# Kernel optimization log

Hardware: AMD Instinct MI355X
Metric: run time of the kernel (lower is better)

Reference implementation:

```python
import jax, jax.numpy as jnp
import numpy as np

EMB, HID, VOC, NLAYERS, TLEN = 256, 512, 32000, 2, 64
SRC_LEN, BS = 128, 64
DEC_HID = 2 * HID  # decoder hidden = hidden_dim * 2


def _p(key, shape, scale=0.05):
    return jax.random.normal(key, shape, dtype=jnp.float32) * scale


def setup_inputs() -> dict:
    key = jax.random.key(0)
    ks = jax.random.split(key, 24)
    d = {}
    d["sentences"] = jax.random.randint(ks[0], (SRC_LEN, BS), 0, VOC)
    d["targets"] = jax.random.randint(ks[1], (TLEN, BS), 0, VOC)
    d["emb"] = _p(ks[2], (VOC, EMB))
    # encoder: bidirectional, 2 layers; gate order i,f,g,o (PyTorch)
    d["enc0_Wih"] = _p(ks[3], (2, 4 * HID, EMB))
    d["enc0_Whh"] = _p(ks[4], (2, 4 * HID, HID))
    d["enc0_bih"] = _p(ks[5], (2, 4 * HID))
    d["enc0_bhh"] = _p(ks[6], (2, 4 * HID))
    d["enc1_Wih"] = _p(ks[7], (2, 4 * HID, 2 * HID))
    d["enc1_Whh"] = _p(ks[8], (2, 4 * HID, HID))
    d["enc1_bih"] = _p(ks[9], (2, 4 * HID))
    d["enc1_bhh"] = _p(ks[10], (2, 4 * HID))
    # decoder: unidirectional, 2 layers, hidden DEC_HID
    d["dec0_Wih"] = _p(ks[11], (4 * DEC_HID, EMB))
    d["dec0_Whh"] = _p(ks[12], (4 * DEC_HID, DEC_HID))
    d["dec0_bih"] = _p(ks[13], (4 * DEC_HID,))
    d["dec0_bhh"] = _p(ks[14], (4 * DEC_HID,))
    d["dec1_Wih"] = _p(ks[15], (4 * DEC_HID, DEC_HID))
    d["dec1_Whh"] = _p(ks[16], (4 * DEC_HID, DEC_HID))
    d["dec1_bih"] = _p(ks[17], (4 * DEC_HID,))
    d["dec1_bhh"] = _p(ks[18], (4 * DEC_HID,))
    d["W_out"] = _p(ks[19], (VOC, DEC_HID))
    d["b_out"] = _p(ks[20], (VOC,))
    return d


def lstm_scan(x, h0, c0, Wih, Whh, bih, bhh, reverse=False):
    # x: (T,B,In). Precompute input projection for the whole sequence.
    xw = jnp.einsum('tbi,gi->tbg', x, Wih) + bih  # (T,B,4H)

    def step(carry, g_in):
        h, c = carry
        g = g_in + h @ Whh.T + bhh
        i, f, gg, o = jnp.split(g, 4, axis=-1)
        c = jax.nn.sigmoid(f) * c + jax.nn.sigmoid(i) * jnp.tanh(gg)
        h = jax.nn.sigmoid(o) * jnp.tanh(c)
        return (h, c), h

    (hT, cT), ys = jax.lax.scan(step, (h0, c0), xw, reverse=reverse)
    return ys, hT, cT


def _forward(sentences, targets, emb,
             enc0_Wih, enc0_Whh, enc0_bih, enc0_bhh,
             enc1_Wih, enc1_Whh, enc1_bih, enc1_bhh,
             dec0_Wih, dec0_Whh, dec0_bih, dec0_bhh,
             dec1_Wih, dec1_Whh, dec1_bih, dec1_bhh,
             W_out, b_out):
    bs = sentences.shape[1]
    x = emb[sentences]  # (S,B,E)
    z = jnp.zeros((bs, HID), jnp.float32)
    enc_layers = ((enc0_Wih, enc0_Whh, enc0_bih, enc0_bhh),
                  (enc1_Wih, enc1_Whh, enc1_bih, enc1_bhh))
    hs, cs = [], []
    for Wih, Whh, bih, bhh in enc_layers:
        yf, hf, cf = lstm_scan(x, z, z, Wih[0], Whh[0], bih[0], bhh[0])
        yb, hb, cb = lstm_scan(x, z, z, Wih[1], Whh[1], bih[1], bhh[1], reverse=True)
        x = jnp.concatenate([yf, yb], axis=-1)  # (S,B,2H)
        hs.append(jnp.concatenate([hf, hb], axis=-1))  # _reshape_hidden concat
        cs.append(jnp.concatenate([cf, cb], axis=-1))
    # teacher forcing: decoder inputs are last source token, then targets[:-1]
    dec_tokens = jnp.concatenate([sentences[-1:], targets[:-1]], axis=0)  # (T,B)
    y = emb[dec_tokens]  # (T,B,E); dropout is identity in eval mode
    dec_layers = ((dec0_Wih, dec0_Whh, dec0_bih, dec0_bhh),
                  (dec1_Wih, dec1_Whh, dec1_bih, dec1_bhh))
    for l, (Wih, Whh, bih, bhh) in enumerate(dec_layers):
        y, _, _ = lstm_scan(y, hs[l], cs[l], Wih, Whh, bih, bhh)
    logits = jnp.einsum('tbh,vh->tbv', y, W_out) + b_out  # (T,B,V)
    return jax.nn.log_softmax(logits, axis=-1)


def reference(sentences, targets, emb,
              enc0_Wih, enc0_Whh, enc0_bih, enc0_bhh,
              enc1_Wih, enc1_Whh, enc1_bih, enc1_bhh,
              dec0_Wih, dec0_Whh, dec0_bih, dec0_bhh,
              dec1_Wih, dec1_Whh, dec1_bih, dec1_bhh,
              W_out, b_out):
    return _forward(sentences, targets, emb,
                    enc0_Wih, enc0_Whh, enc0_bih, enc0_bhh,
                    enc1_Wih, enc1_Whh, enc1_bih, enc1_bhh,
                    dec0_Wih, dec0_Whh, dec0_bih, dec0_bhh,
                    dec1_Wih, dec1_Whh, dec1_bih, dec1_bhh,
                    W_out, b_out)
```

## Files before the change

### kernel.cpp

```cpp
#include <hip/hip_runtime.h>

#define S_LEN 128
#define T_LEN 64
#define BSZ   64
#define EMBD  256
#define HID_  512
#define DHID_ 1024
#define VOC_  32000
#define HSTR  1024

typedef float  f4_t  __attribute__((ext_vector_type(4)));
typedef float  f32x4 __attribute__((ext_vector_type(4)));
typedef short  s16x8 __attribute__((ext_vector_type(8)));
typedef __bf16 bf16x8 __attribute__((ext_vector_type(8)));
typedef unsigned short u16x4 __attribute__((ext_vector_type(4)));
typedef int    i32x2 __attribute__((ext_vector_type(2)));

#define WS_XWA  0ull
#define WS_XWB  (WS_XWA + 16777216ull)
#define WS_CS   (WS_XWB + 16777216ull)
#define WS_BAR  (WS_CS  + 131072ull)
#define WS_BF   (WS_BAR + 32768ull)
#define U_X0B   0ull
#define U_HE0   (U_X0B + 2097152ull)
#define U_HE1   (U_HE0 + 8388608ull)
#define U_HD0   (U_HE1 + 8388608ull)
#define U_HD1   (U_HD0 + 4194304ull)
#define U_HSB   (U_HD1 + 4194304ull)
#define U_E0W   (U_HSB + 131072ull)
#define U_E1W   (U_E0W + 1048576ull)
#define U_D0W   (U_E1W + 4194304ull)
#define U_D1W   (U_D0W + 1048576ull)

__device__ __forceinline__ unsigned short f2bf(float x) {
    unsigned u = __builtin_bit_cast(unsigned, x);
    return (unsigned short)((u + 0x7fffu + ((u >> 16) & 1u)) >> 16);
}

__device__ __forceinline__ f4_t sc_load4(const void* p) {
    f4_t v;
    asm volatile("global_load_dwordx4 %0, %1, off sc0 sc1" : "=v"(v) : "v"(p));
    return v;
}
__device__ __forceinline__ int sc_load1(const int* p) {
    int v;
    asm volatile("global_load_dword %0, %1, off sc0 sc1\n\ts_waitcnt vmcnt(0)"
                 : "=v"(v) : "v"(p) : "memory");
    return v;
}
__device__ __forceinline__ void sc_store_int(int* p, int v) {
    asm volatile("global_store_dword %0, %1, off sc0 sc1" :: "v"(p), "v"(v) : "memory");
}
__device__ __forceinline__ void sc_store8(void* p, i32x2 v) {
    asm volatile("global_store_dwordx2 %0, %1, off sc0 sc1" :: "v"(p), "v"(v) : "memory");
}
__device__ __forceinline__ float g_load1(const float* p) {
    float v;
    asm volatile("global_load_dword %0, %1, off" : "=v"(v) : "v"(p));
    return v;
}
__device__ __forceinline__ void wait_vm0() {
    asm volatile("s_waitcnt vmcnt(0)" ::: "memory");
}
__device__ __forceinline__ void wait_vm8() {
    asm volatile("s_waitcnt vmcnt(8)" ::: "memory");
}

__device__ __forceinline__ void gload_lds16(const void* g, void* l) {
    __builtin_amdgcn_global_load_lds(
        (const __attribute__((address_space(1))) void*)g,
        (__attribute__((address_space(3))) void*)l, 16, 0, 0);
}

__device__ __forceinline__ float sigmoidf_(float x) { return 1.f / (1.f + expf(-x)); }

__global__ __launch_bounds__(256) void f2b_kernel(
    const float* __restrict__ in, unsigned short* __restrict__ out, int n4)
{
    const int stride = gridDim.x * 256;
    for (int i = blockIdx.x * 256 + threadIdx.x; i < n4; i += stride) {
        const float4 v = reinterpret_cast<const float4*>(in)[i];
        u16x4 o = { f2bf(v.x), f2bf(v.y), f2bf(v.z), f2bf(v.w) };
        reinterpret_cast<u16x4*>(out)[i] = o;
    }
}

__global__ __launch_bounds__(64) void embed_src_kernel(
    const int* __restrict__ toks, const float* __restrict__ emb,
    unsigned short* __restrict__ out)
{
    const int i = blockIdx.x;
    const int tok = toks[i];
    const float4 v = reinterpret_cast<const float4*>(emb + (size_t)tok * EMBD)[threadIdx.x];
    u16x4 o = { f2bf(v.x), f2bf(v.y), f2bf(v.z), f2bf(v.w) };
    reinterpret_cast<u16x4*>(out + (size_t)i * EMBD)[threadIdx.x] = o;
}

__global__ __launch_bounds__(64) void embed_dec_kernel(
    const int* __restrict__ sent, const int* __restrict__ targ,
    const float* __restrict__ emb, unsigned short* __restrict__ out)
{
    const int i = blockIdx.x;
    const int t = i >> 6, b = i & 63;
    const int tok = (t == 0) ? sent[(S_LEN - 1) * BSZ + b] : targ[(t - 1) * BSZ + b];
    const float4 v = reinterpret_cast<const float4*>(emb + (size_t)tok * EMBD)[threadIdx.x];
    u16x4 o = { f2bf(v.x), f2bf(v.y), f2bf(v.z), f2bf(v.w) };
    reinterpret_cast<u16x4*>(out + (size_t)i * EMBD)[threadIdx.x] = o;
}

__global__ __launch_bounds__(256) void gemm_bf16_kernel(
    const unsigned short* __restrict__ A, const unsigned short* __restrict__ B,
    const float* __restrict__ b1, const float* __restrict__ b2,
    float* __restrict__ C, int M, int N, int K, int nTN, int tmode)
{
    __shared__ __align__(16) unsigned short As[128 * 64];
    __shared__ __align__(16) unsigned short Bs[128 * 64];

    const int tid  = threadIdx.x;
    const int lane = tid & 63;
    const int wv   = tid >> 6;
    const int wm   = wv >> 1, wn = wv & 1;

    const int nwg = gridDim.x;
    const int q = nwg >> 3, r = nwg & 7;
    const int xcd = blockIdx.x & 7, io = blockIdx.x >> 3;
    const int wg = (xcd < r ? xcd * (q + 1) : r * (q + 1) + (xcd - r) * q) + io;
    const int bm = (wg / nTN) * 128;
    const int bn = (wg % nTN) * 128;

    f32x4 acc[4][4];
#pragma unroll
    for (int i = 0; i < 4; ++i)
#pragma unroll
        for (int j = 0; j < 4; ++j) acc[i][j] = (f32x4)0.f;

    const int lin_base = wv * 1024 + lane * 16;

    for (int k0 = 0; k0 < K; k0 += 64) {
        __syncthreads();
#pragma unroll
        for (int qc = 0; qc < 4; ++qc) {
            const int lin = qc * 4096 + lin_base;
            const int row = lin >> 7;
            const int c   = (lin >> 4) & 7;
            const int sc  = c ^ (row & 7);
            const size_t gofs  = (size_t)(bm + row) * K + k0 + sc * 8;
            const size_t gofsB = (size_t)(bn + row) * K + k0 + sc * 8;
            char* ldst  = (char*)As + qc * 4096 + wv * 1024;
            char* ldstB = (char*)Bs + qc * 4096 + wv * 1024;
            gload_lds16(A + gofs, ldst);
            gload_lds16(B + gofsB, ldstB);
        }
        asm volatile("s_waitcnt vmcnt(0)" ::: "memory");
        __syncthreads();
#pragma unroll
        for (int ks = 0; ks < 2; ++ks) {
            bf16x8 af[4], bfv[4];
            const int ca = ks * 4 + (lane >> 4);
#pragma unroll
            for (int f = 0; f < 4; ++f) {
                const int ra = wm * 64 + f * 16 + (lane & 15);
                af[f] = __builtin_bit_cast(bf16x8,
                    *(const s16x8*)((const char*)As + ra * 128 + ((ca ^ (ra & 7)) << 4)));
                const int rb = wn * 64 + f * 16 + (lane & 15);
                bfv[f] = __builtin_bit_cast(bf16x8,
                    *(const s16x8*)((const char*)Bs + rb * 128 + ((ca ^ (rb & 7)) << 4)));
            }
#pragma unroll
            for (int i = 0; i < 4; ++i)
#pragma unroll
                for (int j = 0; j < 4; ++j)
                    acc[i][j] = __builtin_amdgcn_mfma_f32_16x16x32_bf16(
                        af[i], bfv[j], acc[i][j], 0, 0, 0);
        }
    }

    const int col0 = bn + wn * 64 + (lane & 15);
    if (tmode == 0) {
        const int row0 = bm + wm * 64 + ((lane >> 4) << 2);
#pragma unroll
        for (int i = 0; i < 4; ++i) {
#pragma unroll
            for (int j = 0; j < 4; ++j) {
                const int col = col0 + j * 16;
                float bias = b1[col];
                if (b2) bias += b2[col];
#pragma unroll
                for (int rg = 0; rg < 4; ++rg)
                    C[(size_t)(row0 + i * 16 + rg) * N + col] = acc[i][j][rg] + bias;
            }
        }
    } else {
        const int tblk = (bm >> 6) + wm;
        const int rb = (lane >> 4) << 2;
#pragma unroll
        for (int i = 0; i < 4; ++i) {
#pragma unroll
            for (int j = 0; j < 4; ++j) {
                const int col = col0 + j * 16;
                float bias = b1[col];
                if (b2) bias += b2[col];
                float4 v = { acc[i][j][0] + bias, acc[i][j][1] + bias,
                             acc[i][j][2] + bias, acc[i][j][3] + bias };
                *reinterpret_cast<float4*>(&C[((size_t)tblk * N + col) * 64 + rb + i * 16]) = v;
            }
        }
    }
}

template<int H_T>
__global__ __launch_bounds__(256, 1) void lstm_mfma_scan(
    const float* __restrict__ xw0, const float* __restrict__ xw1,
    const float* __restrict__ Whh0, const float* __restrict__ Whh1,
    const unsigned short* __restrict__ h0b, const float* __restrict__ c0,
    unsigned short* __restrict__ hist,
    unsigned short* __restrict__ hsb, float* __restrict__ csd,
    int T, int ndir, int rev_mask, int* bar)
{
    constexpr int KST = H_T / 32;
    constexpr int CH  = H_T / 8;
    constexpr int NB  = CH / 32;

    __shared__ __align__(16) unsigned short h_lds[64 * H_T];
    __shared__ float pre[64][17];
    __shared__ __align__(8) unsigned short hpack[64][4];

    const int tid  = threadIdx.x;
    const int lane = tid & 63;
    const int w    = tid >> 6;
    const int bpd  = (ndir == 2) ? 128 : 256;
    const int dir  = blockIdx.x / bpd;
    const int blk  = blockIdx.x - dir * bpd;
    const int m0   = blk * 4;
    const int rev  = (rev_mask >> dir) & 1;
    const float* xw  = dir ? xw1  : xw0;
    const float* Whh = dir ? Whh1 : Whh0;
    const int dcol = dir * H_T;
    const int b = tid & 63;
    const int j = tid >> 6;

    int* myflag = bar + blockIdx.x * 32;
    const int* pollflag = bar + (dir * bpd + (tid < bpd ? tid : 0)) * 32;
    const bool polls = (tid < bpd);

    const int n  = lane & 15;
    const int kg = lane >> 4;
    const int wr = (n >> 2) * H_T + m0 + (n & 3);
    s16x8 wfr[KST];
#pragma unroll
    for (int ks = 0; ks < KST; ++ks) {
        const float* wp = Whh + (size_t)wr * H_T + ks * 32 + kg * 8;
        const float4 lo = *reinterpret_cast<const float4*>(wp);
        const float4 hi = *reinterpret_cast<const float4*>(wp + 4);
        s16x8 rr;
        rr[0] = (short)f2bf(lo.x); rr[1] = (short)f2bf(lo.y);
        rr[2] = (short)f2bf(lo.z); rr[3] = (short)f2bf(lo.w);
        rr[4] = (short)f2bf(hi.x); rr[5] = (short)f2bf(hi.y);
        rr[6] = (short)f2bf(hi.z); rr[7] = (short)f2bf(hi.w);
        wfr[ks] = rr;
    }

    float c  = c0 ? c0[(size_t)b * HSTR + dcol + m0 + j] : 0.f;
    float hn = 0.f;
    const int rA = w * 16 + n;
    const int rAx = rA & 7;

    for (int s = 0; s < T; ++s) {
        const int tt = rev ? (T - 1 - s) : s;

        const float* xb = xw + ((size_t)tt * (4 * H_T) + m0 + j) * 64 + b;
        float xg0 = g_load1(xb);
        float xg1 = g_load1(xb + (size_t)H_T * 64);
        float xg2 = g_load1(xb + (size_t)2 * H_T * 64);
        float xg3 = g_load1(xb + (size_t)3 * H_T * 64);

        if (s > 0) {
            int ok = polls ? 0 : 1;
            for (;;) {
                if (!ok) ok = (sc_load1(pollflag) >= s) ? 1 : 0;
                if (__syncthreads_and(ok)) break;
            }
        }

        const unsigned short* hb;
        size_t tofs;
        if (s == 0) { hb = h0b; tofs = 0; }
        else {
            const int tp = rev ? (tt + 1) : (tt - 1);
            hb = hist; tofs = (size_t)tp * (64 * 1024);
        }

        float p0 = 0.f, p1 = 0.f, p2 = 0.f, p3 = 0.f;
        if (hb) {
            f4_t bufA[8], bufB[8];
            auto issue = [&](f4_t (&bf)[8], int bt) {
#pragma unroll
                for (int jj = 0; jj < 8; ++jj) {
                    const int idx = (bt * 8 + jj) * 256 + tid;
                    const int rr_ = idx / CH, cc_ = idx % CH;
                    bf[jj] = sc_load4(hb + tofs + (size_t)rr_ * 1024 + dcol + cc_ * 8);
                }
            };
            auto writeb = [&](const f4_t (&bf)[8], int bt) {
#pragma unroll
                for (int jj = 0; jj < 8; ++jj) {
                    const int idx = (bt * 8 + jj) * 256 + tid;
                    const int rr_ = idx / CH, cc_ = idx % CH;
                    const int off = rr_ * (2 * H_T) + ((cc_ ^ (rr_ & 7)) << 4);
                    *(f4_t*)((char*)h_lds + off) = bf[jj];
                }
            };
            issue(bufA, 0);
            if (NB > 1) issue(bufB, 1);
#pragma unroll
            for (int bt = 0; bt < NB; ++bt) {
                if (bt + 1 < NB) wait_vm8(); else wait_vm0();
                if (bt & 1) writeb(bufB, bt); else writeb(bufA, bt);
                if (bt + 2 < NB) { if (bt & 1) issue(bufB, bt + 2); else issue(bufA, bt + 2); }
            }
            __syncthreads();

            f32x4 acc = {0.f, 0.f, 0.f, 0.f};
#pragma unroll
            for (int ks = 0; ks < KST; ++ks) {
                const int cc_ = ks * 4 + kg;
                const int off = rA * (2 * H_T) + ((cc_ ^ rAx) << 4);
                const bf16x8 a = __builtin_bit_cast(bf16x8,
                    *(const s16x8*)((const char*)h_lds + off));
                acc = __builtin_amdgcn_mfma_f32_16x16x32_bf16(
                    a, __builtin_bit_cast(bf16x8, wfr[ks]), acc, 0, 0, 0);
            }
            __syncthreads();
#pragma unroll
            for (int rg = 0; rg < 4; ++rg)
                pre[w * 16 + kg * 4 + rg][n] = acc[rg];
            __syncthreads();
            p0 = pre[b][0 + j]; p1 = pre[b][4 + j];
            p2 = pre[b][8 + j]; p3 = pre[b][12 + j];
        }

        asm volatile("s_waitcnt vmcnt(0)"
                     : "+v"(xg0), "+v"(xg1), "+v"(xg2), "+v"(xg3) :: "memory");

        const float ig = sigmoidf_(p0 + xg0);
        const float fg = sigmoidf_(p1 + xg1);
        const float gg = tanhf(p2 + xg2);
        const float og = sigmoidf_(p3 + xg3);
        c  = fg * c + ig * gg;
        hn = og * tanhf(c);

        hpack[b][j] = f2bf(hn);
        __syncthreads();
        if (tid < 64) {
            const i32x2 v2 = *reinterpret_cast<const i32x2*>(&hpack[tid][0]);
            sc_store8(hist + (size_t)tt * (64 * 1024) + (size_t)tid * 1024 + dcol + m0, v2);
        }
        wait_vm0();
        __syncthreads();
        if (s + 1 < T && tid == 0) sc_store_int(myflag, s + 1);
    }

    if (hsb) hsb[(size_t)b * 1024 + dcol + m0 + j] = f2bf(hn);
    if (csd) csd[(size_t)b * HSTR + dcol + m0 + j] = c;
}

__global__ __launch_bounds__(256) void logsoftmax_kernel(float* __restrict__ x, int n4)
{
    const int tid = threadIdx.x;
    float4* p = reinterpret_cast<float4*>(x + (size_t)blockIdx.x * (n4 * 4));
    float m = -3.0e38f, s = 0.f;
    for (int cc = tid; cc < n4; cc += 256) {
        const float4 v = p[cc];
        const float vv[4] = { v.x, v.y, v.z, v.w };
#pragma unroll
        for (int e = 0; e < 4; ++e) {
            const float z = vv[e];
            if (z > m) { s = s * expf(m - z) + 1.f; m = z; }
            else       { s += expf(z - m); }
        }
    }
    __shared__ float ms[256], ss[256];
    ms[tid] = m; ss[tid] = s;
    __syncthreads();
    for (int off = 128; off > 0; off >>= 1) {
        if (tid < off) {
            const float m2 = ms[tid + off], s2 = ss[tid + off];
            const float m1 = ms[tid],       s1 = ss[tid];
            const float M = fmaxf(m1, m2);
            ss[tid] = s1 * expf(m1 - M) + s2 * expf(m2 - M);
            ms[tid] = M;
        }
        __syncthreads();
    }
    const float ML = ms[0] + logf(ss[0]);
    for (int cc = tid; cc < n4; cc += 256) {
        float4 v = p[cc];
        v.x -= ML; v.y -= ML; v.z -= ML; v.w -= ML;
        p[cc] = v;
    }
}

extern "C" void kernel_launch(void* const* d_in, const int* in_sizes, int n_in,
                              void* d_out, int out_size, void* d_ws, size_t ws_size,
                              hipStream_t stream)
{
    const int*   sent  = (const int*)d_in[0];
    const int*   targ  = (const int*)d_in[1];
    const float* emb   = (const float*)d_in[2];
    const float* e0Wih = (const float*)d_in[3];
    const float* e0Whh = (const float*)d_in[4];
    const float* e0bih = (const float*)d_in[5];
    const float* e0bhh = (const float*)d_in[6];
    const float* e1Wih = (const float*)d_in[7];
    const float* e1Whh = (const float*)d_in[8];
    const float* e1bih = (const float*)d_in[9];
    const float* e1bhh = (const float*)d_in[10];
    const float* d0Wih = (const float*)d_in[11];
    const float* d0Whh = (const float*)d_in[12];
    const float* d0bih = (const float*)d_in[13];
    const float* d0bhh = (const float*)d_in[14];
    const float* d1Wih = (const float*)d_in[15];
    const float* d1Whh = (const float*)d_in[16];
    const float* d1bih = (const float*)d_in[17];
    const float* d1bhh = (const float*)d_in[18];
    const float* Wout  = (const float*)d_in[19];
    const float* bout  = (const float*)d_in[20];

    float* ws  = (float*)d_ws;
    float* xwA = ws + WS_XWA;
    float* xwB = ws + WS_XWB;
    float* cs  = ws + WS_CS;
    int*   bar = (int*)(ws + WS_BAR);
    unsigned short* ub    = (unsigned short*)(ws + WS_BF);
    unsigned short* x0b   = ub + U_X0B;
    unsigned short* h_e0  = ub + U_HE0;
    unsigned short* h_e1  = ub + U_HE1;
    unsigned short* h_d0  = ub + U_HD0;
    unsigned short* h_d1  = ub + U_HD1;
    unsigned short* hsb   = ub + U_HSB;
    unsigned short* e0Wb  = ub + U_E0W;
    unsigned short* e1Wb  = ub + U_E1W;
    unsigned short* d0Wb  = ub + U_D0W;
    unsigned short* d1Wb  = ub + U_D1W;
    unsigned short* Woutb = (unsigned short*)xwA;
    float* out = (float*)d_out;

    hipMemsetAsync(bar, 0, 4 * 8192 * sizeof(int), stream);

    f2b_kernel<<<256, 256, 0, stream>>>(e0Wih, e0Wb, 1048576 / 4);
    f2b_kernel<<<512, 256, 0, stream>>>(e1Wih, e1Wb, 4194304 / 4);
    f2b_kernel<<<256, 256, 0, stream>>>(d0Wih, d0Wb, 1048576 / 4);
    f2b_kernel<<<512, 256, 0, stream>>>(d1Wih, d1Wb, 4194304 / 4);

    embed_src_kernel<<<S_LEN * BSZ, 64, 0, stream>>>(sent, emb, x0b);
    gemm_bf16_kernel<<<64 * 16, 256, 0, stream>>>(x0b, e0Wb, e0bih, e0bhh, xwA,
                                                  S_LEN * BSZ, 2048, EMBD, 16, 1);
    gemm_bf16_kernel<<<64 * 16, 256, 0, stream>>>(x0b, e0Wb + 2048ull * 256,
                                                  e0bih + 2048, e0bhh + 2048, xwB,
                                                  S_LEN * BSZ, 2048, EMBD, 16, 1);
    lstm_mfma_scan<512><<<256, 256, 0, stream>>>(xwA, xwB, e0Whh, e0Whh + 2048ull * 512,
                                                 nullptr, nullptr, h_e0,
                                                 hsb, cs, S_LEN, 2, 2, bar);
    gemm_bf16_kernel<<<64 * 16, 256, 0, stream>>>(h_e0, e1Wb, e1bih, e1bhh, xwA,
                                                  S_LEN * BSZ, 2048, 2 * HID_, 16, 1);
    gemm_bf16_kernel<<<64 * 16, 256, 0, stream>>>(h_e0, e1Wb + 2048ull * 1024,
                                                  e1bih + 2048, e1bhh + 2048, xwB,
                                                  S_LEN * BSZ, 2048, 2 * HID_, 16, 1);
    lstm_mfma_scan<512><<<256, 256, 0, stream>>>(xwA, xwB, e1Whh, e1Whh + 2048ull * 512,
                                                 nullptr, nullptr, h_e1,
                                                 hsb + 65536, cs + 65536,
                                                 S_LEN, 2, 2, bar + 8192);
    embed_dec_kernel<<<T_LEN * BSZ, 64, 0, stream>>>(sent, targ, emb, x0b);
    gemm_bf16_kernel<<<32 * 32, 256, 0, stream>>>(x0b, d0Wb, d0bih, d0bhh, xwA,
                                                  T_LEN * BSZ, 4 * DHID_, EMBD, 32, 1);
    lstm_mfma_scan<1024><<<256, 256, 0, stream>>>(xwA, nullptr, d0Whh, nullptr,
                                                  hsb, cs, h_d0,
                                                  nullptr, nullptr, T_LEN, 1, 0,
                                                  bar + 2 * 8192);
    f2b_kernel<<<2048, 256, 0, stream>>>(Wout, Woutb, (VOC_ * DHID_) / 4);
    gemm_bf16_kernel<<<32 * 32, 256, 0, stream>>>(h_d0, d1Wb, d1bih, d1bhh, xwB,
                                                  T_LEN * BSZ, 4 * DHID_, DHID_, 32, 1);
    lstm_mfma_scan<1024><<<256, 256, 0, stream>>>(xwB, nullptr, d1Whh, nullptr,
                                                  hsb + 65536, cs + 65536, h_d1,
                                                  nullptr, nullptr, T_LEN, 1, 0,
                                                  bar + 3 * 8192);
    gemm_bf16_kernel<<<32 * 250, 256, 0, stream>>>(h_d1, Woutb, bout, nullptr, out,
                                                   T_LEN * BSZ, VOC_, DHID_, 250, 0);
    logsoftmax_kernel<<<T_LEN * BSZ, 256, 0, stream>>>(out, VOC_ / 4);
}
```

Before: 2.711 ms.

## Pack more LSTM cells per block and store gate preactivations as bf16

The persistent LSTM scan now runs fewer, larger blocks: 512 threads each handling 16 or 8 cells instead of 4. This cuts the number of blocks taking part in the per-step cross-block flag barrier, at the cost of each block pulling more of the h state into LDS every step. The input-projection GEMM now writes bf16 instead of fp32, halving the xw buffer that the scan reads. The scan also prefetches the next step's xw values right after the barrier flag is set, overlapping those loads with the wait. Wout conversion is moved to the front, and the workspace is laid out again so the bf16 buffers no longer alias.

```diff
diff --git a/kernel.cpp b/kernel.cpp
--- a/kernel.cpp
+++ b/kernel.cpp
@@ -16,25 +16,29 @@
 typedef unsigned short u16x4 __attribute__((ext_vector_type(4)));
 typedef int    i32x2 __attribute__((ext_vector_type(2)));
 
-#define WS_XWA  0ull
-#define WS_XWB  (WS_XWA + 16777216ull)
-#define WS_CS   (WS_XWB + 16777216ull)
-#define WS_BAR  (WS_CS  + 131072ull)
+#define WS_CS   0ull
+#define WS_BAR  (WS_CS + 131072ull)
 #define WS_BF   (WS_BAR + 32768ull)
 #define U_X0B   0ull
-#define U_HE0   (U_X0B + 2097152ull)
-#define U_HE1   (U_HE0 + 8388608ull)
-#define U_HD0   (U_HE1 + 8388608ull)
-#define U_HD1   (U_HD0 + 4194304ull)
-#define U_HSB   (U_HD1 + 4194304ull)
-#define U_E0W   (U_HSB + 131072ull)
-#define U_E1W   (U_E0W + 1048576ull)
-#define U_D0W   (U_E1W + 4194304ull)
-#define U_D1W   (U_D0W + 1048576ull)
+#define U_HE0   (U_X0B  + 2097152ull)
+#define U_HE1   (U_HE0  + 8388608ull)
+#define U_HD0   (U_HE1  + 8388608ull)
+#define U_HD1   (U_HD0  + 4194304ull)
+#define U_HSB   (U_HD1  + 4194304ull)
+#define U_E0W   (U_HSB  + 131072ull)
+#define U_E1W   (U_E0W  + 1048576ull)
+#define U_D0W   (U_E1W  + 4194304ull)
+#define U_D1W   (U_D0W  + 1048576ull)
+#define U_XWA   (U_D1W  + 4194304ull)
+#define U_XWB   (U_XWA  + 16777216ull)
+#define U_WOUT  (U_XWB  + 16777216ull)
 
 __device__ __forceinline__ unsigned short f2bf(float x) {
     unsigned u = __builtin_bit_cast(unsigned, x);
     return (unsigned short)((u + 0x7fffu + ((u >> 16) & 1u)) >> 16);
+}
+__device__ __forceinline__ float bf2f(unsigned u) {
+    return __builtin_bit_cast(float, u << 16);
 }
 
 __device__ __forceinline__ f4_t sc_load4(const void* p) {
@@ -54,16 +58,16 @@
 __device__ __forceinline__ void sc_store8(void* p, i32x2 v) {
     asm volatile("global_store_dwordx2 %0, %1, off sc0 sc1" :: "v"(p), "v"(v) : "memory");
 }
-__device__ __forceinline__ float g_load1(const float* p) {
-    float v;
-    asm volatile("global_load_dword %0, %1, off" : "=v"(v) : "v"(p));
+__device__ __forceinline__ unsigned g_load_us(const unsigned short* p) {
+    unsigned v;
+    asm volatile("global_load_ushort %0, %1, off" : "=v"(v) : "v"(p));
     return v;
 }
 __device__ __forceinline__ void wait_vm0() {
     asm volatile("s_waitcnt vmcnt(0)" ::: "memory");
 }
-__device__ __forceinline__ void wait_vm8() {
-    asm volatile("s_waitcnt vmcnt(8)" ::: "memory");
+__device__ __forceinline__ void wait_vm4() {
+    asm volatile("s_waitcnt vmcnt(4)" ::: "memory");
 }
 
 __device__ __forceinline__ void gload_lds16(const void* g, void* l) {
@@ -111,7 +115,7 @@
 __global__ __launch_bounds__(256) void gemm_bf16_kernel(
     const unsigned short* __restrict__ A, const unsigned short* __restrict__ B,
     const float* __restrict__ b1, const float* __restrict__ b2,
-    float* __restrict__ C, int M, int N, int K, int nTN, int tmode)
+    void* __restrict__ Cv, int M, int N, int K, int nTN, int tmode)
 {
     __shared__ __align__(16) unsigned short As[128 * 64];
     __shared__ __align__(16) unsigned short Bs[128 * 64];
@@ -177,6 +181,7 @@
 
     const int col0 = bn + wn * 64 + (lane & 15);
     if (tmode == 0) {
+        float* C = (float*)Cv;
         const int row0 = bm + wm * 64 + ((lane >> 4) << 2);
 #pragma unroll
         for (int i = 0; i < 4; ++i) {
@@ -191,6 +196,7 @@
             }
         }
     } else {
+        unsigned short* C = (unsigned short*)Cv;
         const int tblk = (bm >> 6) + wm;
         const int rb = (lane >> 4) << 2;
 #pragma unroll
@@ -200,79 +206,105 @@
                 const int col = col0 + j * 16;
                 float bias = b1[col];
                 if (b2) bias += b2[col];
-                float4 v = { acc[i][j][0] + bias, acc[i][j][1] + bias,
-                             acc[i][j][2] + bias, acc[i][j][3] + bias };
-                *reinterpret_cast<float4*>(&C[((size_t)tblk * N + col) * 64 + rb + i * 16]) = v;
-            }
-        }
-    }
-}
-
-template<int H_T>
-__global__ __launch_bounds__(256, 1) void lstm_mfma_scan(
-    const float* __restrict__ xw0, const float* __restrict__ xw1,
+                u16x4 o = { f2bf(acc[i][j][0] + bias), f2bf(acc[i][j][1] + bias),
+                            f2bf(acc[i][j][2] + bias), f2bf(acc[i][j][3] + bias) };
+                *reinterpret_cast<u16x4*>(&C[((size_t)tblk * N + col) * 64 + rb + i * 16]) = o;
+            }
+        }
+    }
+}
+
+template<int H_T, int CELLS>
+__global__ __launch_bounds__(512, 1) void lstm_mfma_scan(
+    const unsigned short* __restrict__ xw0, const unsigned short* __restrict__ xw1,
     const float* __restrict__ Whh0, const float* __restrict__ Whh1,
     const unsigned short* __restrict__ h0b, const float* __restrict__ c0,
     unsigned short* __restrict__ hist,
     unsigned short* __restrict__ hsb, float* __restrict__ csd,
     int T, int ndir, int rev_mask, int* bar)
 {
-    constexpr int KST = H_T / 32;
-    constexpr int CH  = H_T / 8;
-    constexpr int NB  = CH / 32;
+    constexpr int KST   = H_T / 32;
+    constexpr int CH    = H_T / 8;
+    constexpr int NB    = (64 * CH) / 2048;
+    constexpr int NGQ   = CELLS / 8;
+    constexpr int PAIRS = CELLS / 8;
+    constexpr int CH8   = CELLS / 4;
 
     __shared__ __align__(16) unsigned short h_lds[64 * H_T];
-    __shared__ float pre[64][17];
-    __shared__ __align__(8) unsigned short hpack[64][4];
+    __shared__ float pre[4][CELLS][65];
+    __shared__ __align__(8) unsigned short hpack[64][CELLS + 4];
 
     const int tid  = threadIdx.x;
     const int lane = tid & 63;
     const int w    = tid >> 6;
-    const int bpd  = (ndir == 2) ? 128 : 256;
+    const int bq   = w & 3;
+    const int gh   = w >> 2;
+    const int n    = lane & 15;
+    const int kg   = lane >> 4;
+    const int bpd  = H_T / CELLS;
     const int dir  = blockIdx.x / bpd;
     const int blk  = blockIdx.x - dir * bpd;
-    const int m0   = blk * 4;
+    const int m0c  = blk * CELLS;
     const int rev  = (rev_mask >> dir) & 1;
-    const float* xw  = dir ? xw1  : xw0;
+    const unsigned short* xw = dir ? xw1 : xw0;
     const float* Whh = dir ? Whh1 : Whh0;
     const int dcol = dir * H_T;
-    const int b = tid & 63;
-    const int j = tid >> 6;
 
     int* myflag = bar + blockIdx.x * 32;
     const int* pollflag = bar + (dir * bpd + (tid < bpd ? tid : 0)) * 32;
     const bool polls = (tid < bpd);
 
-    const int n  = lane & 15;
-    const int kg = lane >> 4;
-    const int wr = (n >> 2) * H_T + m0 + (n & 3);
-    s16x8 wfr[KST];
-#pragma unroll
-    for (int ks = 0; ks < KST; ++ks) {
-        const float* wp = Whh + (size_t)wr * H_T + ks * 32 + kg * 8;
-        const float4 lo = *reinterpret_cast<const float4*>(wp);
-        const float4 hi = *reinterpret_cast<const float4*>(wp + 4);
-        s16x8 rr;
-        rr[0] = (short)f2bf(lo.x); rr[1] = (short)f2bf(lo.y);
-        rr[2] = (short)f2bf(lo.z); rr[3] = (short)f2bf(lo.w);
-        rr[4] = (short)f2bf(hi.x); rr[5] = (short)f2bf(hi.y);
-        rr[6] = (short)f2bf(hi.z); rr[7] = (short)f2bf(hi.w);
-        wfr[ks] = rr;
-    }
-
-    float c  = c0 ? c0[(size_t)b * HSTR + dcol + m0 + j] : 0.f;
-    float hn = 0.f;
-    const int rA = w * 16 + n;
+    s16x8 wfr[NGQ][KST];
+#pragma unroll
+    for (int qq = 0; qq < NGQ; ++qq) {
+        int g, cc;
+        if constexpr (CELLS == 16) { g = 2 * gh + qq; cc = n; }
+        else                       { g = 2 * gh + (n >> 3); cc = n & 7; }
+        const size_t wr = (size_t)(g * H_T + m0c + cc) * H_T;
+#pragma unroll
+        for (int ks = 0; ks < KST; ++ks) {
+            const float* wp = Whh + wr + ks * 32 + kg * 8;
+            const float4 lo = *reinterpret_cast<const float4*>(wp);
+            const float4 hi = *reinterpret_cast<const float4*>(wp + 4);
+            s16x8 rr;
+            rr[0] = (short)f2bf(lo.x); rr[1] = (short)f2bf(lo.y);
+            rr[2] = (short)f2bf(lo.z); rr[3] = (short)f2bf(lo.w);
+            rr[4] = (short)f2bf(hi.x); rr[5] = (short)f2bf(hi.y);
+            rr[6] = (short)f2bf(hi.z); rr[7] = (short)f2bf(hi.w);
+            wfr[qq][ks] = rr;
+        }
+    }
+
+    float cst[PAIRS];
+    unsigned xg[PAIRS * 4];
+#pragma unroll
+    for (int i = 0; i < PAIRS; ++i) {
+        const int p = tid + i * 512;
+        const int b_ = p & 63, ci = p >> 6;
+        cst[i] = c0 ? c0[(size_t)b_ * HSTR + dcol + m0c + ci] : 0.f;
+    }
+
+    auto issue_xg = [&](int ttn) {
+#pragma unroll
+        for (int i = 0; i < PAIRS; ++i) {
+            const int p = tid + i * 512;
+            const int b_ = p & 63, ci = p >> 6;
+#pragma unroll
+            for (int g = 0; g < 4; ++g)
+                xg[i * 4 + g] = g_load_us(
+                    xw + ((size_t)ttn * (4 * H_T) + g * H_T + m0c + ci) * 64 + b_);
+        }
+    };
+
+    const int rA  = bq * 16 + n;
     const int rAx = rA & 7;
+    float hnv[PAIRS];
+
+    issue_xg(rev ? (T - 1) : 0);
+    wait_vm0();
 
     for (int s = 0; s < T; ++s) {
         const int tt = rev ? (T - 1 - s) : s;
-
-        const float* xb = xw + ((size_t)tt * (4 * H_T) + m0 + j) * 64 + b;
-        float xg0 = g_load1(xb);
-        float xg1 = g_load1(xb + (size_t)H_T * 64);
-        float xg2 = g_load1(xb + (size_t)2 * H_T * 64);
-        float xg3 = g_load1(xb + (size_t)3 * H_T * 64);
 
         if (s > 0) {
             int ok = polls ? 0 : 1;
@@ -290,21 +322,26 @@
             hb = hist; tofs = (size_t)tp * (64 * 1024);
         }
 
-        float p0 = 0.f, p1 = 0.f, p2 = 0.f, p3 = 0.f;
+        float p_[4][PAIRS];
+#pragma unroll
+        for (int g = 0; g < 4; ++g)
+#pragma unroll
+            for (int i = 0; i < PAIRS; ++i) p_[g][i] = 0.f;
+
         if (hb) {
-            f4_t bufA[8], bufB[8];
-            auto issue = [&](f4_t (&bf)[8], int bt) {
-#pragma unroll
-                for (int jj = 0; jj < 8; ++jj) {
-                    const int idx = (bt * 8 + jj) * 256 + tid;
+            f4_t bufA[4], bufB[4];
+            auto issue = [&](f4_t (&bf)[4], int bt) {
+#pragma unroll
+                for (int jj = 0; jj < 4; ++jj) {
+                    const int idx = (bt * 4 + jj) * 512 + tid;
                     const int rr_ = idx / CH, cc_ = idx % CH;
                     bf[jj] = sc_load4(hb + tofs + (size_t)rr_ * 1024 + dcol + cc_ * 8);
                 }
             };
-            auto writeb = [&](const f4_t (&bf)[8], int bt) {
-#pragma unroll
-                for (int jj = 0; jj < 8; ++jj) {
-                    const int idx = (bt * 8 + jj) * 256 + tid;
+            auto writeb = [&](const f4_t (&bf)[4], int bt) {
+#pragma unroll
+                for (int jj = 0; jj < 4; ++jj) {
+                    const int idx = (bt * 4 + jj) * 512 + tid;
                     const int rr_ = idx / CH, cc_ = idx % CH;
                     const int off = rr_ * (2 * H_T) + ((cc_ ^ (rr_ & 7)) << 4);
                     *(f4_t*)((char*)h_lds + off) = bf[jj];
@@ -314,54 +351,88 @@
             if (NB > 1) issue(bufB, 1);
 #pragma unroll
             for (int bt = 0; bt < NB; ++bt) {
-                if (bt + 1 < NB) wait_vm8(); else wait_vm0();
+                if (bt + 1 < NB) wait_vm4(); else wait_vm0();
                 if (bt & 1) writeb(bufB, bt); else writeb(bufA, bt);
                 if (bt + 2 < NB) { if (bt & 1) issue(bufB, bt + 2); else issue(bufA, bt + 2); }
             }
             __syncthreads();
 
-            f32x4 acc = {0.f, 0.f, 0.f, 0.f};
+            f32x4 acc[NGQ];
+#pragma unroll
+            for (int qq = 0; qq < NGQ; ++qq) acc[qq] = (f32x4)0.f;
 #pragma unroll
             for (int ks = 0; ks < KST; ++ks) {
                 const int cc_ = ks * 4 + kg;
                 const int off = rA * (2 * H_T) + ((cc_ ^ rAx) << 4);
                 const bf16x8 a = __builtin_bit_cast(bf16x8,
                     *(const s16x8*)((const char*)h_lds + off));
-                acc = __builtin_amdgcn_mfma_f32_16x16x32_bf16(
-                    a, __builtin_bit_cast(bf16x8, wfr[ks]), acc, 0, 0, 0);
+#pragma unroll
+                for (int qq = 0; qq < NGQ; ++qq)
+                    acc[qq] = __builtin_amdgcn_mfma_f32_16x16x32_bf16(
+                        a, __builtin_bit_cast(bf16x8, wfr[qq][ks]), acc[qq], 0, 0, 0);
+            }
+#pragma unroll
+            for (int qq = 0; qq < NGQ; ++qq) {
+                int g, cc;
+                if constexpr (CELLS == 16) { g = 2 * gh + qq; cc = n; }
+                else                       { g = 2 * gh + (n >> 3); cc = n & 7; }
+#pragma unroll
+                for (int rg = 0; rg < 4; ++rg)
+                    pre[g][cc][bq * 16 + kg * 4 + rg] = acc[qq][rg];
             }
             __syncthreads();
 #pragma unroll
-            for (int rg = 0; rg < 4; ++rg)
-                pre[w * 16 + kg * 4 + rg][n] = acc[rg];
-            __syncthreads();
-            p0 = pre[b][0 + j]; p1 = pre[b][4 + j];
-            p2 = pre[b][8 + j]; p3 = pre[b][12 + j];
-        }
-
-        asm volatile("s_waitcnt vmcnt(0)"
-                     : "+v"(xg0), "+v"(xg1), "+v"(xg2), "+v"(xg3) :: "memory");
-
-        const float ig = sigmoidf_(p0 + xg0);
-        const float fg = sigmoidf_(p1 + xg1);
-        const float gg = tanhf(p2 + xg2);
-        const float og = sigmoidf_(p3 + xg3);
-        c  = fg * c + ig * gg;
-        hn = og * tanhf(c);
-
-        hpack[b][j] = f2bf(hn);
+            for (int i = 0; i < PAIRS; ++i) {
+                const int p = tid + i * 512;
+                const int b_ = p & 63, ci = p >> 6;
+                p_[0][i] = pre[0][ci][b_]; p_[1][i] = pre[1][ci][b_];
+                p_[2][i] = pre[2][ci][b_]; p_[3][i] = pre[3][ci][b_];
+            }
+        }
+
+        if constexpr (PAIRS == 2)
+            asm volatile("s_waitcnt vmcnt(0)"
+                : "+v"(xg[0]), "+v"(xg[1]), "+v"(xg[2]), "+v"(xg[3]),
+                  "+v"(xg[4]), "+v"(xg[5]), "+v"(xg[6]), "+v"(xg[7]) :: "memory");
+        else
+            asm volatile("s_waitcnt vmcnt(0)"
+                : "+v"(xg[0]), "+v"(xg[1]), "+v"(xg[2]), "+v"(xg[3]) :: "memory");
+
+#pragma unroll
+        for (int i = 0; i < PAIRS; ++i) {
+            const int p = tid + i * 512;
+            const int b_ = p & 63, ci = p >> 6;
+            const float ig = sigmoidf_(p_[0][i] + bf2f(xg[i * 4 + 0]));
+            const float fg = sigmoidf_(p_[1][i] + bf2f(xg[i * 4 + 1]));
+            const float gg = tanhf   (p_[2][i] + bf2f(xg[i * 4 + 2]));
+            const float og = sigmoidf_(p_[3][i] + bf2f(xg[i * 4 + 3]));
+            cst[i] = fg * cst[i] + ig * gg;
+            hnv[i] = og * tanhf(cst[i]);
+            hpack[b_][ci] = f2bf(hnv[i]);
+        }
         __syncthreads();
-        if (tid < 64) {
-            const i32x2 v2 = *reinterpret_cast<const i32x2*>(&hpack[tid][0]);
-            sc_store8(hist + (size_t)tt * (64 * 1024) + (size_t)tid * 1024 + dcol + m0, v2);
+        if (tid < 64 * CH8) {
+            const int b_ = tid / CH8, ch = tid - b_ * CH8;
+            const i32x2 v2 = *reinterpret_cast<const i32x2*>(&hpack[b_][ch * 4]);
+            sc_store8(hist + (size_t)tt * (64 * 1024) + (size_t)b_ * 1024 + dcol + m0c + ch * 4, v2);
         }
         wait_vm0();
         __syncthreads();
-        if (s + 1 < T && tid == 0) sc_store_int(myflag, s + 1);
-    }
-
-    if (hsb) hsb[(size_t)b * 1024 + dcol + m0 + j] = f2bf(hn);
-    if (csd) csd[(size_t)b * HSTR + dcol + m0 + j] = c;
+        if (s + 1 < T) {
+            if (tid == 0) sc_store_int(myflag, s + 1);
+            issue_xg(rev ? (T - 2 - s) : (s + 1));
+        }
+    }
+
+    if (hsb) {
+#pragma unroll
+        for (int i = 0; i < PAIRS; ++i) {
+            const int p = tid + i * 512;
+            const int b_ = p & 63, ci = p >> 6;
+            hsb[(size_t)b_ * 1024 + dcol + m0c + ci] = f2bf(hnv[i]);
+            csd[(size_t)b_ * HSTR + dcol + m0c + ci] = cst[i];
+        }
+    }
 }
 
 __global__ __launch_bounds__(256) void logsoftmax_kernel(float* __restrict__ x, int n4)
@@ -427,8 +498,6 @@
     const float* bout  = (const float*)d_in[20];
 
     float* ws  = (float*)d_ws;
-    float* xwA = ws + WS_XWA;
-    float* xwB = ws + WS_XWB;
     float* cs  = ws + WS_CS;
     int*   bar = (int*)(ws + WS_BAR);
     unsigned short* ub    = (unsigned short*)(ws + WS_BF);
@@ -442,7 +511,9 @@
     unsigned short* e1Wb  = ub + U_E1W;
     unsigned short* d0Wb  = ub + U_D0W;
     unsigned short* d1Wb  = ub + U_D1W;
-    unsigned short* Woutb = (unsigned short*)xwA;
+    unsigned short* xwA   = ub + U_XWA;
+    unsigned short* xwB   = ub + U_XWB;
+    unsigned short* Woutb = ub + U_WOUT;
     float* out = (float*)d_out;
 
     hipMemsetAsync(bar, 0, 4 * 8192 * sizeof(int), stream);
@@ -451,6 +522,7 @@
     f2b_kernel<<<512, 256, 0, stream>>>(e1Wih, e1Wb, 4194304 / 4);
     f2b_kernel<<<256, 256, 0, stream>>>(d0Wih, d0Wb, 1048576 / 4);
     f2b_kernel<<<512, 256, 0, stream>>>(d1Wih, d1Wb, 4194304 / 4);
+    f2b_kernel<<<2048, 256, 0, stream>>>(Wout, Woutb, (VOC_ * DHID_) / 4);
 
     embed_src_kernel<<<S_LEN * BSZ, 64, 0, stream>>>(sent, emb, x0b);
     gemm_bf16_kernel<<<64 * 16, 256, 0, stream>>>(x0b, e0Wb, e0bih, e0bhh, xwA,
@@ -458,32 +530,31 @@
     gemm_bf16_kernel<<<64 * 16, 256, 0, stream>>>(x0b, e0Wb + 2048ull * 256,
                                                   e0bih + 2048, e0bhh + 2048, xwB,
                                                   S_LEN * BSZ, 2048, EMBD, 16, 1);
-    lstm_mfma_scan<512><<<256, 256, 0, stream>>>(xwA, xwB, e0Whh, e0Whh + 2048ull * 512,
-                                                 nullptr, nullptr, h_e0,
-                                                 hsb, cs, S_LEN, 2, 2, bar);
+    lstm_mfma_scan<512, 16><<<64, 512, 0, stream>>>(xwA, xwB, e0Whh, e0Whh + 2048ull * 512,
+                                                    nullptr, nullptr, h_e0,
+                                                    hsb, cs, S_LEN, 2, 2, bar);
     gemm_bf16_kernel<<<64 * 16, 256, 0, stream>>>(h_e0, e1Wb, e1bih, e1bhh, xwA,
                                                   S_LEN * BSZ, 2048, 2 * HID_, 16, 1);
     gemm_bf16_kernel<<<64 * 16, 256, 0, stream>>>(h_e0, e1Wb + 2048ull * 1024,
                                                   e1bih + 2048, e1bhh + 2048, xwB,
                                                   S_LEN * BSZ, 2048, 2 * HID_, 16, 1);
-    lstm_mfma_scan<512><<<256, 256, 0, stream>>>(xwA, xwB, e1Whh, e1Whh + 2048ull * 512,
-                                                 nullptr, nullptr, h_e1,
-                                                 hsb + 65536, cs + 65536,
-                                                 S_LEN, 2, 2, bar + 8192);
+    lstm_mfma_scan<512, 16><<<64, 512, 0, stream>>>(xwA, xwB, e1Whh, e1Whh + 2048ull * 512,
+                                                    nullptr, nullptr, h_e1,
+                                                    hsb + 65536, cs + 65536,
+                                                    S_LEN, 2, 2, bar + 8192);
     embed_dec_kernel<<<T_LEN * BSZ, 64, 0, stream>>>(sent, targ, emb, x0b);
     gemm_bf16_kernel<<<32 * 32, 256, 0, stream>>>(x0b, d0Wb, d0bih, d0bhh, xwA,
                                                   T_LEN * BSZ, 4 * DHID_, EMBD, 32, 1);
-    lstm_mfma_scan<1024><<<256, 256, 0, stream>>>(xwA, nullptr, d0Whh, nullptr,
-                                                  hsb, cs, h_d0,
-                                                  nullptr, nullptr, T_LEN, 1, 0,
-                                                  bar + 2 * 8192);
-    f2b_kernel<<<2048, 256, 0, stream>>>(Wout, Woutb, (VOC_ * DHID_) / 4);
+    lstm_mfma_scan<1024, 8><<<128, 512, 0, stream>>>(xwA, nullptr, d0Whh, nullptr,
+                                                     hsb, cs, h_d0,
+                                                     nullptr, nullptr, T_LEN, 1, 0,
+                                                     bar + 2 * 8192);
     gemm_bf16_kernel<<<32 * 32, 256, 0, stream>>>(h_d0, d1Wb, d1bih, d1bhh, xwB,
                                                   T_LEN * BSZ, 4 * DHID_, DHID_, 32, 1);
-    lstm_mfma_scan<1024><<<256, 256, 0, stream>>>(xwB, nullptr, d1Whh, nullptr,
-                                                  hsb + 65536, cs + 65536, h_d1,
-                                                  nullptr, nullptr, T_LEN, 1, 0,
-                                                  bar + 3 * 8192);
+    lstm_mfma_scan<1024, 8><<<128, 512, 0, stream>>>(xwB, nullptr, d1Whh, nullptr,
+                                                     hsb + 65536, cs + 65536, h_d1,
+                                                     nullptr, nullptr, T_LEN, 1, 0,
+                                                     bar + 3 * 8192);
     gemm_bf16_kernel<<<32 * 250, 256, 0, stream>>>(h_d1, Woutb, bout, nullptr, out,
                                                    T_LEN * BSZ, VOC_, DHID_, 250, 0);
     logsoftmax_kernel<<<T_LEN * BSZ, 256, 0, stream>>>(out, VOC_ / 4);
```

Result: slower. 2.907 ms (+7.2%).
